# Performance work log

Hardware: AMD Instinct MI355X
Metric: run time of the kernel (lower is better)

Reference implementation:

```python
import jax, jax.numpy as jnp
import numpy as np

N, L, D, H, HIST = 4, 1024, 1024, 16, 128
HD = D // H          # head_dim = 64
SCALE = D ** 0.5     # note: original scales by sqrt(model_dim), not sqrt(head_dim)


def _band_mask():
    # get_mask: tril XOR tril(diag=-history_len) -> True inside the causal band.
    # masked_fill fills where mask is True, so pass the complement (True outside band).
    r = jnp.arange(L)[:, None]
    c = jnp.arange(L)[None, :]
    band = (c <= r) & (c > r - HIST)  # band of width HIST incl. diagonal
    return jnp.broadcast_to(~band, (N, 1, L, L))


def setup_inputs() -> dict:
    key = jax.random.key(0)
    ks = jax.random.split(key, 8)
    s = 0.02
    return {
        "values": jax.random.normal(ks[0], (N, L, D), jnp.float32),
        "keys": jax.random.normal(ks[1], (N, L, D), jnp.float32),
        "query": jax.random.normal(ks[2], (N, L, D), jnp.float32),
        "mask": _band_mask(),
        "Wv": jax.random.normal(ks[3], (HD, HD), jnp.float32) * s,
        "Wk": jax.random.normal(ks[4], (HD, HD), jnp.float32) * s,
        "Wq": jax.random.normal(ks[5], (HD, HD), jnp.float32) * s,
        "Wo": jax.random.normal(ks[6], (D, D), jnp.float32) * s,
        "bo": jax.random.normal(ks[7], (D,), jnp.float32) * s,
    }


def reference(values, keys, query, mask, Wv, Wk, Wq, Wo, bo):
    n, qlen, _ = query.shape
    # split heads and apply per-head linear projections (nn.Linear: x @ W.T)
    v = values.reshape(n, -1, H, HD) @ Wv.T
    k = keys.reshape(n, -1, H, HD) @ Wk.T
    q = query.reshape(n, qlen, H, HD) @ Wq.T
    # full energy [n, h, q, k]
    energy = jnp.einsum('nqhd,nkhd->nhqk', q, k)
    energy = jnp.where(mask, jnp.float32(-1e20), energy)
    scores = jax.nn.softmax(energy / SCALE, axis=-1)
    # NOTE: faithful to original einsum 'nhql,nlhd->nlhd' (reduces over q):
    # attention[n,l,h,d] = (sum_q scores[n,h,q,l]) * v[n,l,h,d]
    attention = jnp.einsum('nhql,nlhd->nlhd', scores, v)
    out = attention.reshape(n, qlen, D) @ Wo.T + bo
    return out
```

## Files before the change

kernel.cpp:

```cpp
#include <hip/hip_runtime.h>
#include <hip/hip_bf16.h>
#include <math.h>


using short8 = __attribute__((ext_vector_type(8))) short;
using f32x4  = __attribute__((ext_vector_type(4))) float;

__device__ __forceinline__ unsigned short f2bf(float x) {
    unsigned u = __float_as_uint(x);
    u += 0x7FFFu + ((u >> 16) & 1u);
    return (unsigned short)(u >> 16);
}

__global__ __launch_bounds__(256) void k_prep(const float* __restrict__ keys,
                                              const float* __restrict__ Wq,
                                              const float* __restrict__ Wk,
                                              const float* __restrict__ Wv,
                                              const float4* __restrict__ Wo4,
                                              unsigned short* __restrict__ kbp,
                                              float* __restrict__ w,
                                              ushort4* __restrict__ wob4,
                                              unsigned short* __restrict__ Mtb,
                                              unsigned short* __restrict__ Wvb) {
    const int b = blockIdx.x, tid = threadIdx.x;
    if (b < 1024) {
        const int tile = b & 15, nh = b >> 4, h = nh & 15, n = nh >> 4;
        const int t0 = tile * 64;
        const float* kbase = keys + ((size_t)(n * 1024 + t0)) * 1024 + h * 64;
        unsigned short* kout = kbp + ((size_t)(nh * 1024 + t0)) * 64;
#pragma unroll
        for (int i = 0; i < 4; ++i) {
            int idx = tid + i * 256;
            int r = idx >> 4, f0 = (idx & 15) * 4;
            float4 kv = *reinterpret_cast<const float4*>(kbase + (size_t)r * 1024 + f0);
            ushort4 ko; ko.x = f2bf(kv.x); ko.y = f2bf(kv.y);
            ko.z = f2bf(kv.z); ko.w = f2bf(kv.w);
            *reinterpret_cast<ushort4*>(kout + (size_t)r * 64 + f0) = ko;
        }
        if (tid < 64) w[b * 64 + tid] = 0.f;
    } else if (b < 2048) {
        int idx = (b - 1024) * 256 + tid;
        float4 v = Wo4[idx];
        ushort4 o; o.x = f2bf(v.x); o.y = f2bf(v.y);
        o.z = f2bf(v.z); o.w = f2bf(v.w);
        wob4[idx] = o;
    } else {
        int idx = (b - 2048) * 256 + tid;
        int e = idx >> 6, f = idx & 63;
        float s = 0.f;
#pragma unroll 8
        for (int d = 0; d < 64; ++d) s = fmaf(Wq[d * 64 + e], Wk[d * 64 + f], s);
        Mtb[f * 64 + e] = f2bf(s * (1.0f / 32.0f));
        Wvb[idx] = f2bf(Wv[idx]);
    }
}

__global__ __launch_bounds__(256) void k_w2(const float* __restrict__ query,
                                            const unsigned short* __restrict__ kbp,
                                            const unsigned short* __restrict__ Mtb,
                                            float* __restrict__ w) {
    __shared__ unsigned short yqA[64 * 72];
    __shared__ float wloc[192];

    const int tid  = threadIdx.x;
    const int b    = blockIdx.x;
    const int tile = b & 15;
    const int nh   = b >> 4;
    const int h    = nh & 15;
    const int n    = nh >> 4;
    const int t0   = tile * 64;

    if (tid < 192) wloc[tid] = 0.f;

    const int wv = tid >> 6, lane = tid & 63;
    const int m = lane & 15, q4 = lane >> 4, ksel = q4 * 8;

    {
        const float* qrow = query + ((size_t)(n * 1024 + t0 + wv * 16 + m)) * 1024 + h * 64;
        short8 af[2];
#pragma unroll
        for (int ch = 0; ch < 2; ++ch) {
            float4 x0 = *reinterpret_cast<const float4*>(qrow + ch * 32 + ksel);
            float4 x1 = *reinterpret_cast<const float4*>(qrow + ch * 32 + ksel + 4);
            short8 a;
            a[0] = (short)f2bf(x0.x); a[1] = (short)f2bf(x0.y);
            a[2] = (short)f2bf(x0.z); a[3] = (short)f2bf(x0.w);
            a[4] = (short)f2bf(x1.x); a[5] = (short)f2bf(x1.y);
            a[6] = (short)f2bf(x1.z); a[7] = (short)f2bf(x1.w);
            af[ch] = a;
        }
        f32x4 acc[4];
#pragma unroll
        for (int fc = 0; fc < 4; ++fc) {
            acc[fc] = f32x4{0.f, 0.f, 0.f, 0.f};
#pragma unroll
            for (int ch = 0; ch < 2; ++ch) {
                short8 bf = *reinterpret_cast<const short8*>(
                    Mtb + (size_t)(fc * 16 + m) * 64 + ch * 32 + ksel);
                acc[fc] = __builtin_amdgcn_mfma_f32_16x16x32_bf16(af[ch], bf, acc[fc], 0, 0, 0);
            }
        }
#pragma unroll
        for (int fc = 0; fc < 4; ++fc)
#pragma unroll
            for (int r = 0; r < 4; ++r)
                yqA[(wv * 16 + q4 * 4 + r) * 72 + fc * 16 + m] = f2bf(acc[fc][r]);
    }
    __syncthreads();

    const unsigned short* ya = &yqA[(wv * 16 + m) * 72];
    short8 af0 = *reinterpret_cast<const short8*>(ya + ksel);
    short8 af1 = *reinterpret_cast<const short8*>(ya + 32 + ksel);

    const unsigned short* kb = kbp + (size_t)nh * 1024 * 64;
    short8 bfr[12][2];
#pragma unroll
    for (int ni = 0; ni < 12; ++ni) {
        int l = t0 - 127 + ni * 16 + m;
        int lc = min(max(l, 0), 1023);
        const unsigned short* kp = kb + (size_t)lc * 64 + ksel;
        bfr[ni][0] = *reinterpret_cast<const short8*>(kp);
        bfr[ni][1] = *reinterpret_cast<const short8*>(kp + 32);
    }

    f32x4 acc[12];
#pragma unroll
    for (int ni = 0; ni < 12; ++ni) {
        acc[ni] = f32x4{0.f, 0.f, 0.f, 0.f};
        acc[ni] = __builtin_amdgcn_mfma_f32_16x16x32_bf16(af0, bfr[ni][0], acc[ni], 0, 0, 0);
        acc[ni] = __builtin_amdgcn_mfma_f32_16x16x32_bf16(af1, bfr[ni][1], acc[ni], 0, 0, 0);
    }

    const int rbase = wv * 16 + q4 * 4;
    float rs[4] = {0.f, 0.f, 0.f, 0.f};
#pragma unroll
    for (int ni = 0; ni < 12; ++ni) {
        const int c = ni * 16 + m;
#pragma unroll
        for (int reg = 0; reg < 4; ++reg) {
            const int rlw = rbase + reg;
            bool valid = (c >= rlw) && (c <= rlw + 127) && (c + t0 >= 127);
            float e = valid ? __expf(acc[ni][reg]) : 0.f;
            acc[ni][reg] = e;
            rs[reg] += e;
        }
    }
#pragma unroll
    for (int reg = 0; reg < 4; ++reg) {
#pragma unroll
        for (int mm = 1; mm < 16; mm <<= 1) rs[reg] += __shfl_xor(rs[reg], mm);
        rs[reg] = 1.0f / rs[reg];
    }
#pragma unroll
    for (int ni = 0; ni < 12; ++ni) {
        float cs = acc[ni][0] * rs[0] + acc[ni][1] * rs[1] +
                   acc[ni][2] * rs[2] + acc[ni][3] * rs[3];
        cs += __shfl_xor(cs, 16);
        cs += __shfl_xor(cs, 32);
        if (lane < 16) atomicAdd(&wloc[ni * 16 + m], cs);
    }
    __syncthreads();

    for (int c = tid; c < 192; c += 256) {
        int l = t0 - 127 + c;
        if (l >= 0 && l < 1024)
            atomicAdd(&w[(size_t)nh * 1024 + l], wloc[c]);
    }
}

__global__ __launch_bounds__(256) void k_ap2(const float* __restrict__ values,
                                             const unsigned short* __restrict__ Wvb,
                                             const float* __restrict__ w,
                                             unsigned short* __restrict__ apb) {
    const int tid = threadIdx.x;
    const long R0 = (long)blockIdx.x * 64;
    const int wv = tid >> 6, lane = tid & 63;
    const int m = lane & 15, ksel = (lane >> 4) * 8;

    const float* va = values + (R0 + wv * 16 + m) * 64;
    short8 af[2];
#pragma unroll
    for (int ch = 0; ch < 2; ++ch) {
        float4 x0 = *reinterpret_cast<const float4*>(va + ch * 32 + ksel);
        float4 x1 = *reinterpret_cast<const float4*>(va + ch * 32 + ksel + 4);
        short8 a;
        a[0] = (short)f2bf(x0.x); a[1] = (short)f2bf(x0.y);
        a[2] = (short)f2bf(x0.z); a[3] = (short)f2bf(x0.w);
        a[4] = (short)f2bf(x1.x); a[5] = (short)f2bf(x1.y);
        a[6] = (short)f2bf(x1.z); a[7] = (short)f2bf(x1.w);
        af[ch] = a;
    }

    f32x4 acc[4];
#pragma unroll
    for (int dc = 0; dc < 4; ++dc) {
        acc[dc] = f32x4{0.f, 0.f, 0.f, 0.f};
#pragma unroll
        for (int ch = 0; ch < 2; ++ch) {
            short8 bf = *reinterpret_cast<const short8*>(
                Wvb + (size_t)(dc * 16 + m) * 64 + ch * 32 + ksel);
            acc[dc] = __builtin_amdgcn_mfma_f32_16x16x32_bf16(af[ch], bf, acc[dc], 0, 0, 0);
        }
    }

    const long rowb = R0 + wv * 16 + (lane >> 4) * 4;
    float wf[4];
#pragma unroll
    for (int reg = 0; reg < 4; ++reg) {
        long rg = rowb + reg;
        int hh = (int)(rg & 15);
        int ll = (int)((rg >> 4) & 1023);
        int nn = (int)(rg >> 14);
        wf[reg] = w[((size_t)(nn * 16 + hh) << 10) + ll];
    }
#pragma unroll
    for (int dc = 0; dc < 4; ++dc)
#pragma unroll
        for (int reg = 0; reg < 4; ++reg)
            apb[(size_t)(rowb + reg) * 64 + dc * 16 + m] = f2bf(acc[dc][reg] * wf[reg]);
}

__global__ __launch_bounds__(256) void k_out_mfma(
    const unsigned short* __restrict__ apb,
    const unsigned short* __restrict__ wob,
    const float* __restrict__ bo,
    float* __restrict__ out) {
    __shared__ unsigned short As[128 * 32];
    __shared__ unsigned short Bs[128 * 32];

    const int tid  = threadIdx.x;
    const int wv   = tid >> 6;
    const int lane = tid & 63;
    const int wy   = wv >> 1, wx = wv & 1;

    const int bx = blockIdx.x & 7;
    const int by = blockIdx.x >> 3;
    const long arow0 = (long)by * 128;
    const int  bcol0 = bx * 128;

    f32x4 acc[4][4];
#pragma unroll
    for (int mi = 0; mi < 4; ++mi)
#pragma unroll
        for (int ni = 0; ni < 4; ++ni) acc[mi][ni] = f32x4{0.f, 0.f, 0.f, 0.f};

    const int r0s = tid >> 2;
    const int kks = (tid & 3) * 8;

    for (int kt = 0; kt < 32; ++kt) {
        const int k0 = kt * 32;
#pragma unroll
        for (int i = 0; i < 2; ++i) {
            const unsigned short* g =
                apb + (arow0 + i * 64 + r0s) * 1024 + k0 + kks;
            __builtin_amdgcn_global_load_lds(
                (const __attribute__((address_space(1))) unsigned int*)g,
                (__attribute__((address_space(3))) unsigned int*)&As[i * 2048 + wv * 512],
                16, 0, 0);
        }
#pragma unroll
        for (int i = 0; i < 2; ++i) {
            const unsigned short* g =
                wob + (size_t)(bcol0 + i * 64 + r0s) * 1024 + k0 + kks;
            __builtin_amdgcn_global_load_lds(
                (const __attribute__((address_space(1))) unsigned int*)g,
                (__attribute__((address_space(3))) unsigned int*)&Bs[i * 2048 + wv * 512],
                16, 0, 0);
        }
        __syncthreads();

        const int koff = (lane >> 4) * 8;
        const int rA = wy * 64 + (lane & 15);
        const int rB = wx * 64 + (lane & 15);
        short8 af[4], bf[4];
#pragma unroll
        for (int mi = 0; mi < 4; ++mi)
            af[mi] = *reinterpret_cast<const short8*>(&As[(rA + mi * 16) * 32 + koff]);
#pragma unroll
        for (int ni = 0; ni < 4; ++ni)
            bf[ni] = *reinterpret_cast<const short8*>(&Bs[(rB + ni * 16) * 32 + koff]);
#pragma unroll
        for (int mi = 0; mi < 4; ++mi)
#pragma unroll
            for (int ni = 0; ni < 4; ++ni)
                acc[mi][ni] = __builtin_amdgcn_mfma_f32_16x16x32_bf16(
                    af[mi], bf[ni], acc[mi][ni], 0, 0, 0);
        __syncthreads();
    }

    const int colb = bcol0 + wx * 64 + (lane & 15);
    const int rowb = (int)arow0 + wy * 64 + (lane >> 4) * 4;
#pragma unroll
    for (int ni = 0; ni < 4; ++ni) {
        const int col = colb + ni * 16;
        const float bias = bo[col];
#pragma unroll
        for (int mi = 0; mi < 4; ++mi) {
            const int row = rowb + mi * 16;
#pragma unroll
            for (int r = 0; r < 4; ++r)
                out[(size_t)(row + r) * 1024 + col] = acc[mi][ni][r] + bias;
        }
    }
}

extern "C" void kernel_launch(void* const* d_in, const int* in_sizes, int n_in,
                              void* d_out, int out_size, void* d_ws, size_t ws_size,
                              hipStream_t stream) {
    const float* values = (const float*)d_in[0];
    const float* keys   = (const float*)d_in[1];
    const float* query  = (const float*)d_in[2];
    const float* Wv     = (const float*)d_in[4];
    const float* Wk     = (const float*)d_in[5];
    const float* Wq     = (const float*)d_in[6];
    const float* Wo     = (const float*)d_in[7];
    const float* bo     = (const float*)d_in[8];
    float* out = (float*)d_out;

    float* w            = (float*)d_ws;
    unsigned short* Mtb = (unsigned short*)(w + 65536);
    unsigned short* Wvb = Mtb + 4096;
    unsigned short* wob = Wvb + 4096;
    unsigned short* kbp = wob + 1024 * 1024;
    unsigned short* apb = kbp + 64 * 1024 * 64;

    k_prep<<<2064, 256, 0, stream>>>(keys, Wq, Wk, Wv, (const float4*)Wo,
                                     kbp, w, (ushort4*)wob, Mtb, Wvb);
    k_w2<<<1024, 256, 0, stream>>>(query, kbp, Mtb, w);
    k_ap2<<<1024, 256, 0, stream>>>(values, Wvb, w, apb);
    k_out_mfma<<<256, 256, 0, stream>>>(apb, wob, bo, out);
}
```

Before: 166.2 us.

## Halve output GEMM tile width to double blocks; interleave K loads with MFMA

```diff
diff --git a/kernel.cpp b/kernel.cpp
--- a/kernel.cpp
+++ b/kernel.cpp
@@ -113,22 +113,19 @@
     short8 af1 = *reinterpret_cast<const short8*>(ya + 32 + ksel);
 
     const unsigned short* kb = kbp + (size_t)nh * 1024 * 64;
-    short8 bfr[12][2];
-#pragma unroll
+
+    f32x4 acc[12];
+#pragma unroll
+    for (int ni = 0; ni < 12; ++ni) acc[ni] = f32x4{0.f, 0.f, 0.f, 0.f};
+#pragma unroll 3
     for (int ni = 0; ni < 12; ++ni) {
         int l = t0 - 127 + ni * 16 + m;
         int lc = min(max(l, 0), 1023);
         const unsigned short* kp = kb + (size_t)lc * 64 + ksel;
-        bfr[ni][0] = *reinterpret_cast<const short8*>(kp);
-        bfr[ni][1] = *reinterpret_cast<const short8*>(kp + 32);
-    }
-
-    f32x4 acc[12];
-#pragma unroll
-    for (int ni = 0; ni < 12; ++ni) {
-        acc[ni] = f32x4{0.f, 0.f, 0.f, 0.f};
-        acc[ni] = __builtin_amdgcn_mfma_f32_16x16x32_bf16(af0, bfr[ni][0], acc[ni], 0, 0, 0);
-        acc[ni] = __builtin_amdgcn_mfma_f32_16x16x32_bf16(af1, bfr[ni][1], acc[ni], 0, 0, 0);
+        short8 b0 = *reinterpret_cast<const short8*>(kp);
+        short8 b1 = *reinterpret_cast<const short8*>(kp + 32);
+        acc[ni] = __builtin_amdgcn_mfma_f32_16x16x32_bf16(af0, b0, acc[ni], 0, 0, 0);
+        acc[ni] = __builtin_amdgcn_mfma_f32_16x16x32_bf16(af1, b1, acc[ni], 0, 0, 0);
     }
 
     const int rbase = wv * 16 + q4 * 4;
@@ -226,21 +223,21 @@
     const float* __restrict__ bo,
     float* __restrict__ out) {
     __shared__ unsigned short As[128 * 32];
-    __shared__ unsigned short Bs[128 * 32];
+    __shared__ unsigned short Bs[64 * 32];
 
     const int tid  = threadIdx.x;
     const int wv   = tid >> 6;
     const int lane = tid & 63;
-    const int wy   = wv >> 1, wx = wv & 1;
-
-    const int bx = blockIdx.x & 7;
-    const int by = blockIdx.x >> 3;
+    const int m    = lane & 15;
+
+    const int bx = blockIdx.x & 15;
+    const int by = blockIdx.x >> 4;
     const long arow0 = (long)by * 128;
-    const int  bcol0 = bx * 128;
-
-    f32x4 acc[4][4];
-#pragma unroll
-    for (int mi = 0; mi < 4; ++mi)
+    const int  bcol0 = bx * 64;
+
+    f32x4 acc[2][4];
+#pragma unroll
+    for (int mi = 0; mi < 2; ++mi)
 #pragma unroll
         for (int ni = 0; ni < 4; ++ni) acc[mi][ni] = f32x4{0.f, 0.f, 0.f, 0.f};
 
@@ -258,29 +255,27 @@
                 (__attribute__((address_space(3))) unsigned int*)&As[i * 2048 + wv * 512],
                 16, 0, 0);
         }
-#pragma unroll
-        for (int i = 0; i < 2; ++i) {
+        {
             const unsigned short* g =
-                wob + (size_t)(bcol0 + i * 64 + r0s) * 1024 + k0 + kks;
+                wob + (size_t)(bcol0 + r0s) * 1024 + k0 + kks;
             __builtin_amdgcn_global_load_lds(
                 (const __attribute__((address_space(1))) unsigned int*)g,
-                (__attribute__((address_space(3))) unsigned int*)&Bs[i * 2048 + wv * 512],
+                (__attribute__((address_space(3))) unsigned int*)&Bs[wv * 512],
                 16, 0, 0);
         }
         __syncthreads();
 
         const int koff = (lane >> 4) * 8;
-        const int rA = wy * 64 + (lane & 15);
-        const int rB = wx * 64 + (lane & 15);
-        short8 af[4], bf[4];
-#pragma unroll
-        for (int mi = 0; mi < 4; ++mi)
+        const int rA = wv * 32 + m;
+        short8 af[2], bf[4];
+#pragma unroll
+        for (int mi = 0; mi < 2; ++mi)
             af[mi] = *reinterpret_cast<const short8*>(&As[(rA + mi * 16) * 32 + koff]);
 #pragma unroll
         for (int ni = 0; ni < 4; ++ni)
-            bf[ni] = *reinterpret_cast<const short8*>(&Bs[(rB + ni * 16) * 32 + koff]);
-#pragma unroll
-        for (int mi = 0; mi < 4; ++mi)
+            bf[ni] = *reinterpret_cast<const short8*>(&Bs[(ni * 16 + m) * 32 + koff]);
+#pragma unroll
+        for (int mi = 0; mi < 2; ++mi)
 #pragma unroll
             for (int ni = 0; ni < 4; ++ni)
                 acc[mi][ni] = __builtin_amdgcn_mfma_f32_16x16x32_bf16(
@@ -288,14 +283,14 @@
         __syncthreads();
     }
 
-    const int colb = bcol0 + wx * 64 + (lane & 15);
-    const int rowb = (int)arow0 + wy * 64 + (lane >> 4) * 4;
+    const int colb = bcol0 + m;
+    const int rowb = (int)arow0 + wv * 32 + (lane >> 4) * 4;
 #pragma unroll
     for (int ni = 0; ni < 4; ++ni) {
         const int col = colb + ni * 16;
         const float bias = bo[col];
 #pragma unroll
-        for (int mi = 0; mi < 4; ++mi) {
+        for (int mi = 0; mi < 2; ++mi) {
             const int row = rowb + mi * 16;
 #pragma unroll
             for (int r = 0; r < 4; ++r)
@@ -328,5 +323,5 @@
                                      kbp, w, (ushort4*)wob, Mtb, Wvb);
     k_w2<<<1024, 256, 0, stream>>>(query, kbp, Mtb, w);
     k_ap2<<<1024, 256, 0, stream>>>(values, Wvb, w, apb);
-    k_out_mfma<<<256, 256, 0, stream>>>(apb, wob, bo, out);
-}
+    k_out_mfma<<<512, 256, 0, stream>>>(apb, wob, bo, out);
+}
```

Result: slower. 200.8 us (+20.8%).
